# Kernel optimization log

Measured on AMD Instinct MI355X. Metric: run time of the kernel, lower is better.

Reference implementation:

```python
import jax, jax.numpy as jnp
import numpy as np

WIDTH = 64
HEIGHT = 64
FEAT = 128
LAT = 64
NUM_SLOTS = 7


def pixel_coords(img_size):
    g = jnp.linspace(-1.0, 1.0, img_size)
    g1, g2 = jnp.meshgrid(g, g, indexing='ij')  # matches torch.meshgrid default
    return jnp.stack([g1, g2], axis=0)[None]  # (1, 2, S, S)


def clamp_pg(x, lo, hi):
    # clamp that preserves gradients (straight-through)
    return x + jax.lax.stop_gradient(jnp.clip(x, lo, hi) - x)


def setup_inputs() -> dict:
    key = jax.random.key(0)
    k0, k1, k2, k3 = jax.random.split(key, 4)
    bs = 64
    x = jax.random.normal(k0, (bs, FEAT, WIDTH, HEIGHT), jnp.float32)
    rand_pixel = jax.random.uniform(k1, (bs, 1, WIDTH, HEIGHT), jnp.float32)
    conv_w = jax.random.normal(k2, (LAT, FEAT), jnp.float32) / np.sqrt(FEAT)
    conv_b = jax.random.normal(k3, (LAT,), jnp.float32) * 0.01
    gate = jnp.asarray(0.5, jnp.float32)  # ScalarGate parameter (nonzero so c_f is non-degenerate)
    # laplacian kernel: sigma_init = 1 / (sqrt(num_slots) * log 2)
    log_sigma = jnp.asarray(np.log(1.0 / (np.sqrt(NUM_SLOTS) * np.log(2.0))), jnp.float32)
    return {'x': x, 'rand_pixel': rand_pixel, 'conv_w': conv_w, 'conv_b': conv_b,
            'gate': gate, 'log_sigma': log_sigma, 'num_cl_steps': 6}


def _forward(x, rand_pixel, conv_w, conv_b, gate, log_sigma, num_cl_steps):
    bs = x.shape[0]
    # SemiConv: gated 1x1 conv + fixed uv coordinate channels
    out = gate * (jnp.einsum('of,bfhw->bohw', conv_w, x) + conv_b[None, :, None, None])
    uv = jnp.concatenate([jnp.zeros((1, LAT - 2, WIDTH, HEIGHT), out.dtype),
                          pixel_coords(WIDTH).astype(out.dtype)], axis=1)
    c_f = out + uv                      # (bs, LAT, W, H)
    delta = out[:, -2:]                 # (bs, 2, W, H)
    sigma = jnp.exp(log_sigma)
    c_flat = c_f.reshape(bs, LAT, -1)   # (bs, LAT, W*H)
    b_idx = jnp.arange(bs)
    log_s0 = jnp.zeros((bs, 1, WIDTH, HEIGHT), c_f.dtype)

    def step(log_s, _):
        # interpolate-to-same-size is identity -> scope = exp(log_s)
        probs = (rand_pixel * jnp.exp(log_s)).reshape(bs, -1)
        idx = jnp.argmax(probs, axis=1)                 # (bs,)
        seed = c_flat[b_idx, :, idx]                    # (bs, LAT)
        diff = c_f - seed[:, :, None, None]
        dist = jnp.sqrt(clamp_pg((diff ** 2).sum(1), 1e-10, 1e10))  # euclidian (laplacian kernel)
        alpha = jnp.exp(-dist / sigma)[:, None]         # (bs, 1, W, H)
        alpha = clamp_pg(alpha, 0.01, 0.99)
        log_m = log_s + jnp.log(alpha)
        new_log_s = log_s + jnp.log1p(-alpha)
        return new_log_s, (log_m, new_log_s, seed)

    log_s_final, (log_m_steps, log_s_steps, seeds) = jax.lax.scan(
        step, log_s0, None, length=num_cl_steps)
    # log_m_k has num_cl_steps masks plus the final scope appended
    log_m_k = jnp.concatenate([log_m_steps, log_s_final[None]], axis=0)
    log_s_k = jnp.concatenate([log_s0[None], log_s_steps], axis=0)
    return log_m_k, log_s_k, c_f, delta, seeds


def reference(x, rand_pixel, conv_w, conv_b, gate, log_sigma, num_cl_steps):
    return _forward(x, rand_pixel, conv_w, conv_b, gate, log_sigma, num_cl_steps)
```

## Files before the change

kernel.cpp:

```cpp
#include <hip/hip_runtime.h>
#include <hip/hip_bf16.h>

#define NPIX 4096
#define FEAT 128
#define LAT 64
#define BS 64
#define NSTEPS 6

#define OFF_LOGM  0u
#define OFF_LOGS  1835008u
#define OFF_CF    3670016u
#define OFF_DELTA 20447232u
#define OFF_SEEDS 20971520u

typedef float f32x4 __attribute__((ext_vector_type(4)));
typedef short s16x8 __attribute__((ext_vector_type(8)));
typedef short s16x4 __attribute__((ext_vector_type(4)));

__device__ __forceinline__ void amax_comb(float& bv, int& bi, float v, int i) {
    if (v > bv || (v == bv && i < bi)) { bv = v; bi = i; }
}

__device__ __forceinline__ short f2bf_rne(float r) {
    __hip_bfloat16 h = __float2bfloat16(r);
    return __builtin_bit_cast(short, h);
}

__device__ __forceinline__ void split2(float v, short& hi, short& lo) {
    unsigned u = __builtin_bit_cast(unsigned, v);
    hi = (short)(u >> 16);
    float hf = __builtin_bit_cast(float, u & 0xFFFF0000u);
    lo = f2bf_rne(v - hf);
}

__device__ __forceinline__ void transpose4(float4& v, int b) {
    float4 w;
    w.x = __shfl_xor(v.x, 1, 64); w.y = __shfl_xor(v.y, 1, 64);
    w.z = __shfl_xor(v.z, 1, 64); w.w = __shfl_xor(v.w, 1, 64);
    float4 u;
    if ((b & 1) == 0) u = make_float4(v.x, w.x, v.z, w.z);
    else              u = make_float4(w.y, v.y, w.w, v.w);
    float4 w2;
    w2.x = __shfl_xor(u.x, 2, 64); w2.y = __shfl_xor(u.y, 2, 64);
    w2.z = __shfl_xor(u.z, 2, 64); w2.w = __shfl_xor(u.w, 2, 64);
    if ((b & 2) == 0) v = make_float4(u.x, u.y, w2.x, w2.y);
    else              v = make_float4(w2.z, w2.w, u.z, u.w);
}

__global__ void prep_w(const float* __restrict__ w, const float* __restrict__ gate_p,
                       short* __restrict__ gwh, short* __restrict__ gwl)
{
    int i = blockIdx.x * 256 + threadIdx.x;
    float v = gate_p[0] * w[i];
    short h, l; split2(v, h, l);
    gwh[i] = h; gwl[i] = l;
}

template<bool PRE>
__global__ __launch_bounds__(256, PRE ? 4 : 2) void conv_mfma(
    const float* __restrict__ x, const float* __restrict__ rand_pixel,
    const float* __restrict__ w, const float* __restrict__ bias,
    const float* __restrict__ gate_p, float* __restrict__ out,
    float* __restrict__ pval, int* __restrict__ pidx, int* __restrict__ cnt,
    const short* __restrict__ gwh, const short* __restrict__ gwl)
{
    __shared__ __align__(16) short Xhi[256][36];
    __shared__ __align__(16) short Xlo[256][36];
    __shared__ __align__(16) short Whi[PRE ? 1 : 64][PRE ? 1 : 136];
    __shared__ __align__(16) short Wlo[PRE ? 1 : 64][PRE ? 1 : 136];
    __shared__ float sbias[64];

    const int tid  = threadIdx.x;
    const int b    = blockIdx.x >> 4;
    const int tile = blockIdx.x & 15;
    const int p0   = tile * 256;
    const int lane = tid & 63;
    const int wv   = tid >> 6;
    const int l15  = lane & 15;
    const int lg   = lane >> 4;

    if (tile == 0 && wv == 0 && lane < 8) cnt[b * 8 + lane] = 0;

    if constexpr (!PRE) {
        const float gate = gate_p[0];
        #pragma unroll
        for (int i = 0; i < 8; ++i) {
            int q = i * 256 + tid;
            int o = q >> 5;
            int f = (q & 31) * 4;
            float4 wq = *(const float4*)(w + o * 128 + f);
            short h0, l0, h1, l1, h2, l2, h3, l3;
            split2(gate * wq.x, h0, l0);
            split2(gate * wq.y, h1, l1);
            split2(gate * wq.z, h2, l2);
            split2(gate * wq.w, h3, l3);
            *(short4*)&Whi[o][f] = make_short4(h0, h1, h2, h3);
            *(short4*)&Wlo[o][f] = make_short4(l0, l1, l2, l3);
        }
    }
    if (tid < 64) sbias[tid] = gate_p[0] * bias[tid];

    f32x4 acc[4][4];
    #pragma unroll
    for (int og = 0; og < 4; ++og)
        #pragma unroll
        for (int pg = 0; pg < 4; ++pg)
            acc[og][pg] = (f32x4){0.f, 0.f, 0.f, 0.f};

    const float* xb = x + (size_t)b * FEAT * NPIX + p0;

    for (int kc = 0; kc < 4; ++kc) {
        __syncthreads();
        const float* xc = xb + (size_t)(kc * 32) * NPIX + (tid & ~3);
        #pragma unroll
        for (int i = 0; i < 8; ++i) {
            float4 v = *(const float4*)(xc + (size_t)(i * 4 + (tid & 3)) * NPIX);
            transpose4(v, tid & 3);
            short h0, l0, h1, l1, h2, l2, h3, l3;
            split2(v.x, h0, l0);
            split2(v.y, h1, l1);
            split2(v.z, h2, l2);
            split2(v.w, h3, l3);
            *(short4*)&Xhi[tid][i * 4] = make_short4(h0, h1, h2, h3);
            *(short4*)&Xlo[tid][i * 4] = make_short4(l0, l1, l2, l3);
        }
        __syncthreads();

        s16x8 Ah[4], Al[4];
        #pragma unroll
        for (int og = 0; og < 4; ++og) {
            if constexpr (PRE) {
                Ah[og] = *(const s16x8*)&gwh[(og * 16 + l15) * 128 + kc * 32 + lg * 8];
                Al[og] = *(const s16x8*)&gwl[(og * 16 + l15) * 128 + kc * 32 + lg * 8];
            } else {
                Ah[og] = *(const s16x8*)&Whi[og * 16 + l15][kc * 32 + lg * 8];
                Al[og] = *(const s16x8*)&Wlo[og * 16 + l15][kc * 32 + lg * 8];
            }
        }

        #pragma unroll
        for (int pg = 0; pg < 4; ++pg) {
            int pxl = wv * 64 + pg * 16 + l15;
            const short* ph = &Xhi[pxl][lg * 8];
            const short* pl = &Xlo[pxl][lg * 8];
            s16x4 h0 = *(const s16x4*)ph, h1 = *(const s16x4*)(ph + 4);
            s16x4 q0 = *(const s16x4*)pl, q1 = *(const s16x4*)(pl + 4);
            s16x8 Bh = {h0[0], h0[1], h0[2], h0[3], h1[0], h1[1], h1[2], h1[3]};
            s16x8 Bl = {q0[0], q0[1], q0[2], q0[3], q1[0], q1[1], q1[2], q1[3]};
            #pragma unroll
            for (int og = 0; og < 4; ++og) {
                acc[og][pg] = __builtin_amdgcn_mfma_f32_16x16x32_bf16(Ah[og], Bh, acc[og][pg], 0, 0, 0);
                acc[og][pg] = __builtin_amdgcn_mfma_f32_16x16x32_bf16(Ah[og], Bl, acc[og][pg], 0, 0, 0);
                acc[og][pg] = __builtin_amdgcn_mfma_f32_16x16x32_bf16(Al[og], Bh, acc[og][pg], 0, 0, 0);
            }
        }
    }

    float* cf = out + OFF_CF + (size_t)b * LAT * NPIX;
    #pragma unroll
    for (int og = 0; og < 4; ++og) {
        #pragma unroll
        for (int pg = 0; pg < 4; ++pg) {
            #pragma unroll
            for (int r = 0; r < 4; ++r) {
                int o = og * 16 + lg * 4 + r;
                int p = p0 + wv * 64 + pg * 16 + l15;
                float v = acc[og][pg][r] + sbias[o];
                if (o == 62) {
                    out[OFF_DELTA + ((size_t)b * 2 + 0) * NPIX + p] = v;
                    v += (float)(-1.0 + 2.0 * (double)(p >> 6) / 63.0);
                } else if (o == 63) {
                    out[OFF_DELTA + ((size_t)b * 2 + 1) * NPIX + p] = v;
                    v += (float)(-1.0 + 2.0 * (double)(p & 63) / 63.0);
                }
                cf[(size_t)o * NPIX + p] = v;
            }
        }
    }

    if (wv == 0) {
        *(float4*)(out + OFF_LOGS + (size_t)b * NPIX + p0 + lane * 4) =
            make_float4(0.f, 0.f, 0.f, 0.f);
        float4 rv = *(const float4*)(rand_pixel + (size_t)b * NPIX + p0 + lane * 4);
        int pb = p0 + lane * 4;
        float bv = rv.x; int bi = pb;
        if (rv.y > bv) { bv = rv.y; bi = pb + 1; }
        if (rv.z > bv) { bv = rv.z; bi = pb + 2; }
        if (rv.w > bv) { bv = rv.w; bi = pb + 3; }
        #pragma unroll
        for (int off = 32; off > 0; off >>= 1) {
            float ov = __shfl_down(bv, off, 64);
            int   oi = __shfl_down(bi, off, 64);
            amax_comb(bv, bi, ov, oi);
        }
        if (lane == 0) { pval[blockIdx.x] = bv; pidx[blockIdx.x] = bi; }
    }
}

#define REP16(OP) OP(0) OP(1) OP(2) OP(3) OP(4) OP(5) OP(6) OP(7) \
                  OP(8) OP(9) OP(10) OP(11) OP(12) OP(13) OP(14) OP(15)

__global__ __launch_bounds__(1024) void steps_fused(
    const float* __restrict__ rand_pixel, const float* __restrict__ log_sigma_p,
    float* __restrict__ out, float* pv, int* pi, int* cnt)
{
    __shared__ float s_mv[16];
    __shared__ int   s_mi[16];
    __shared__ __align__(16) float s_seed[LAT];
    __shared__ float s_rv[16];
    __shared__ int   s_ri[16];

    const int tid  = threadIdx.x;
    const int b    = blockIdx.x >> 2;
    const int tile = blockIdx.x & 3;
    const int p    = tile * 1024 + tid;

    const float* cfb = out + OFF_CF + (size_t)b * LAT * NPIX;

#define DECLR(i) f32x4 r##i;
    REP16(DECLR)
#define LOADR(i) { \
        float4 v = *(const float4*)(cfb + (size_t)(4*i + (tid & 3)) * NPIX + tile * 1024 + (tid & ~3)); \
        transpose4(v, tid & 3); \
        r##i = (f32x4){v.x, v.y, v.z, v.w}; }
    REP16(LOADR)

    f32x4 aq = r0 * r0;
#define SQR(i) aq += r##i * r##i;
    SQR(1) SQR(2) SQR(3) SQR(4) SQR(5) SQR(6) SQR(7)
    SQR(8) SQR(9) SQR(10) SQR(11) SQR(12) SQR(13) SQR(14) SQR(15)
    const float cr2 = aq[0] + aq[1] + aq[2] + aq[3];

    const float rp    = rand_pixel[(size_t)b * NPIX + p];
    const float sigma = expf(log_sigma_p[0]);
    float ls = 0.f;

    #pragma unroll 1
    for (int s = 0; s < NSTEPS; ++s) {
        if (s > 0) {
            if (tid == 0) {
                while (__hip_atomic_load(&cnt[b * 8 + s], __ATOMIC_ACQUIRE,
                                         __HIP_MEMORY_SCOPE_AGENT) < 4)
                    __builtin_amdgcn_s_sleep(2);
            }
            __syncthreads();
        }
        const int nmerge = (s == 0) ? 16 : 4;
        if (tid < nmerge) {
            s_mv[tid] = __hip_atomic_load(&pv[(s * BS + b) * 16 + tid],
                                          __ATOMIC_RELAXED, __HIP_MEMORY_SCOPE_AGENT);
            s_mi[tid] = __hip_atomic_load(&pi[(s * BS + b) * 16 + tid],
                                          __ATOMIC_RELAXED, __HIP_MEMORY_SCOPE_AGENT);
        }
        __syncthreads();

        float bv = -1.0f; int bi = 0;
        for (int k = 0; k < nmerge; ++k) amax_comb(bv, bi, s_mv[k], s_mi[k]);

        if (tid < LAT) s_seed[tid] = cfb[(size_t)tid * NPIX + bi];
        __syncthreads();
        if (tile == 0 && tid < LAT)
            out[OFF_SEEDS + ((size_t)s * BS + b) * LAT + tid] = s_seed[tid];

        f32x4 dacc = (f32x4){0.f, 0.f, 0.f, 0.f};
        f32x4 sacc = (f32x4){0.f, 0.f, 0.f, 0.f};
#define DOT(i) { f32x4 sv = *(const f32x4*)&s_seed[4*i]; dacc += r##i * sv; sacc += sv * sv; }
        REP16(DOT)
        float dot = dacc[0] + dacc[1] + dacc[2] + dacc[3];
        float s2  = sacc[0] + sacc[1] + sacc[2] + sacc[3];
        float d2  = cr2 + s2 - 2.0f * dot;

        float dist  = sqrtf(fminf(fmaxf(d2, 1e-10f), 1e10f));
        float alpha = expf(-dist / sigma);
        alpha = fminf(fmaxf(alpha, 0.01f), 0.99f);
        float lm  = ls + logf(alpha);
        float lsn = ls + log1pf(-alpha);

        out[OFF_LOGM + ((size_t)s * BS + b) * NPIX + p]       = lm;
        out[OFF_LOGS + ((size_t)(s + 1) * BS + b) * NPIX + p] = lsn;
        ls = lsn;

        if (s == NSTEPS - 1) {
            out[OFF_LOGM + ((size_t)NSTEPS * BS + b) * NPIX + p] = lsn;
        } else {
            float prob = rp * expf(lsn);
            int   idx  = p;
            #pragma unroll
            for (int off = 32; off > 0; off >>= 1) {
                float ov = __shfl_down(prob, off, 64);
                int   oi = __shfl_down(idx, off, 64);
                amax_comb(prob, idx, ov, oi);
            }
            int lane = tid & 63, wid = tid >> 6;
            if (lane == 0) { s_rv[wid] = prob; s_ri[wid] = idx; }
            __syncthreads();
            if (tid == 0) {
                float fb = s_rv[0]; int fi = s_ri[0];
                #pragma unroll
                for (int k = 1; k < 16; ++k) amax_comb(fb, fi, s_rv[k], s_ri[k]);
                __hip_atomic_store(&pv[((s + 1) * BS + b) * 16 + tile], fb,
                                   __ATOMIC_RELAXED, __HIP_MEMORY_SCOPE_AGENT);
                __hip_atomic_store(&pi[((s + 1) * BS + b) * 16 + tile], fi,
                                   __ATOMIC_RELAXED, __HIP_MEMORY_SCOPE_AGENT);
                __hip_atomic_fetch_add(&cnt[b * 8 + s + 1], 1,
                                       __ATOMIC_RELEASE, __HIP_MEMORY_SCOPE_AGENT);
            }
        }
    }
}

__global__ __launch_bounds__(1024) void step_kernel(
    const float* __restrict__ rand_pixel, const float* __restrict__ log_sigma_p,
    float* __restrict__ out, float* pv, int* pi, int step)
{
    __shared__ float s_mv[16];
    __shared__ int   s_mi[16];
    __shared__ __align__(16) float s_seed[LAT];
    __shared__ float s_rv[16];
    __shared__ int   s_ri[16];

    const int tid  = threadIdx.x;
    const int b    = blockIdx.x >> 2;
    const int tile = blockIdx.x & 3;
    const int p    = tile * 1024 + tid;

    const float* cfb = out + OFF_CF + (size_t)b * LAT * NPIX;

    const int nmerge = (step == 0) ? 16 : 4;
    if (tid < nmerge) { s_mv[tid] = pv[(step * BS + b) * 16 + tid];
                        s_mi[tid] = pi[(step * BS + b) * 16 + tid]; }
    __syncthreads();
    float bv = -1.0f; int bi = 0;
    for (int k = 0; k < nmerge; ++k) amax_comb(bv, bi, s_mv[k], s_mi[k]);

    if (tid < LAT) s_seed[tid] = cfb[(size_t)tid * NPIX + bi];
    __syncthreads();
    if (tile == 0 && tid < LAT)
        out[OFF_SEEDS + ((size_t)step * BS + b) * LAT + tid] = s_seed[tid];

    float d2 = 0.f;
    #pragma unroll
    for (int c = 0; c < LAT; ++c) {
        float d = cfb[(size_t)c * NPIX + p] - s_seed[c];
        d2 = fmaf(d, d, d2);
    }
    float dist  = sqrtf(fminf(fmaxf(d2, 1e-10f), 1e10f));
    float sigma = expf(log_sigma_p[0]);
    float alpha = expf(-dist / sigma);
    alpha = fminf(fmaxf(alpha, 0.01f), 0.99f);

    float ls  = out[OFF_LOGS + ((size_t)step * BS + b) * NPIX + p];
    float lm  = ls + logf(alpha);
    float lsn = ls + log1pf(-alpha);

    out[OFF_LOGM + ((size_t)step * BS + b) * NPIX + p]       = lm;
    out[OFF_LOGS + ((size_t)(step + 1) * BS + b) * NPIX + p] = lsn;
    if (step == NSTEPS - 1)
        out[OFF_LOGM + ((size_t)NSTEPS * BS + b) * NPIX + p] = lsn;

    if (step < NSTEPS - 1) {
        float prob = rand_pixel[(size_t)b * NPIX + p] * expf(lsn);
        int   idx  = p;
        #pragma unroll
        for (int off = 32; off > 0; off >>= 1) {
            float ov = __shfl_down(prob, off, 64);
            int   oi = __shfl_down(idx, off, 64);
            amax_comb(prob, idx, ov, oi);
        }
        int lane = tid & 63, wid = tid >> 6;
        if (lane == 0) { s_rv[wid] = prob; s_ri[wid] = idx; }
        __syncthreads();
        if (tid == 0) {
            float fb = s_rv[0]; int fi = s_ri[0];
            #pragma unroll
            for (int k = 1; k < 16; ++k) amax_comb(fb, fi, s_rv[k], s_ri[k]);
            pv[((step + 1) * BS + b) * 16 + tile] = fb;
            pi[((step + 1) * BS + b) * 16 + tile] = fi;
        }
    }
}

extern "C" void kernel_launch(void* const* d_in, const int* in_sizes, int n_in,
                              void* d_out, int out_size, void* d_ws, size_t ws_size,
                              hipStream_t stream) {
    const float* x          = (const float*)d_in[0];
    const float* rand_pixel = (const float*)d_in[1];
    const float* w          = (const float*)d_in[2];
    const float* bias       = (const float*)d_in[3];
    const float* gate       = (const float*)d_in[4];
    const float* log_sigma  = (const float*)d_in[5];

    float* out = (float*)d_out;
    float* pv  = (float*)d_ws;
    int*   pi  = (int*)((char*)d_ws + 24576);
    int*   cnt = (int*)((char*)d_ws + 49152);
    short* gwh = (short*)((char*)d_ws + 51200);
    short* gwl = (short*)((char*)d_ws + 67584);

    const bool pre = (ws_size >= 100 * 1024);

    if (pre) {
        prep_w<<<32, 256, 0, stream>>>(w, gate, gwh, gwl);
        conv_mfma<true><<<1024, 256, 0, stream>>>(x, rand_pixel, w, bias, gate, out,
                                                  pv, pi, cnt, gwh, gwl);
    } else {
        conv_mfma<false><<<1024, 256, 0, stream>>>(x, rand_pixel, w, bias, gate, out,
                                                   pv, pi, cnt, nullptr, nullptr);
    }

    const float* a0 = rand_pixel; const float* a1 = log_sigma; float* a2 = out;
    float* a3 = pv; int* a4 = pi; int* a5 = cnt;
    void* kp[6] = {(void*)&a0, (void*)&a1, (void*)&a2, (void*)&a3, (void*)&a4, (void*)&a5};
    hipError_t e = hipLaunchCooperativeKernel((const void*)steps_fused,
                                              dim3(256), dim3(1024), kp, 0, stream);
    if (e != hipSuccess) {
        for (int s = 0; s < NSTEPS; ++s)
            step_kernel<<<256, 1024, 0, stream>>>(rand_pixel, log_sigma, out, pv, pi, s);
    }
}
```

Before: 145.6 us.

## Load conv inputs directly into registers with double-buffered prefetch, drop LDS staging

The conv kernel no longer stages the transposed, hi/lo-split activations through shared memory. Each lane loads its own float4 fragments straight from global memory into a two-deep register buffer, prefetches the next K chunk while the current one is being computed, and does the transpose and bf16 split in registers right before the MFMAs. This removes the per-chunk LDS writes, reads and barriers, at the cost of more registers and a launch bound dropped to 2 waves per SIMD for the prepacked path. The non-prepacked fallback is removed, so the code now assumes the workspace is large enough. The steps kernel also switches its c_f loads to scalar strided loads instead of float4 loads with a shuffle transpose.

```diff
diff --git a/kernel.cpp b/kernel.cpp
--- a/kernel.cpp
+++ b/kernel.cpp
@@ -15,7 +15,6 @@
 
 typedef float f32x4 __attribute__((ext_vector_type(4)));
 typedef short s16x8 __attribute__((ext_vector_type(8)));
-typedef short s16x4 __attribute__((ext_vector_type(4)));
 
 __device__ __forceinline__ void amax_comb(float& bv, int& bi, float v, int i) {
     if (v > bv || (v == bv && i < bi)) { bv = v; bi = i; }
@@ -56,18 +55,13 @@
     gwh[i] = h; gwl[i] = l;
 }
 
-template<bool PRE>
-__global__ __launch_bounds__(256, PRE ? 4 : 2) void conv_mfma(
+__global__ __launch_bounds__(256, 2) void conv_mfma(
     const float* __restrict__ x, const float* __restrict__ rand_pixel,
-    const float* __restrict__ w, const float* __restrict__ bias,
-    const float* __restrict__ gate_p, float* __restrict__ out,
+    const float* __restrict__ bias, const float* __restrict__ gate_p,
+    float* __restrict__ out,
     float* __restrict__ pval, int* __restrict__ pidx, int* __restrict__ cnt,
     const short* __restrict__ gwh, const short* __restrict__ gwl)
 {
-    __shared__ __align__(16) short Xhi[256][36];
-    __shared__ __align__(16) short Xlo[256][36];
-    __shared__ __align__(16) short Whi[PRE ? 1 : 64][PRE ? 1 : 136];
-    __shared__ __align__(16) short Wlo[PRE ? 1 : 64][PRE ? 1 : 136];
     __shared__ float sbias[64];
 
     const int tid  = threadIdx.x;
@@ -78,26 +72,9 @@
     const int wv   = tid >> 6;
     const int l15  = lane & 15;
     const int lg   = lane >> 4;
+    const int j    = l15 & 3;
 
     if (tile == 0 && wv == 0 && lane < 8) cnt[b * 8 + lane] = 0;
-
-    if constexpr (!PRE) {
-        const float gate = gate_p[0];
-        #pragma unroll
-        for (int i = 0; i < 8; ++i) {
-            int q = i * 256 + tid;
-            int o = q >> 5;
-            int f = (q & 31) * 4;
-            float4 wq = *(const float4*)(w + o * 128 + f);
-            short h0, l0, h1, l1, h2, l2, h3, l3;
-            split2(gate * wq.x, h0, l0);
-            split2(gate * wq.y, h1, l1);
-            split2(gate * wq.z, h2, l2);
-            split2(gate * wq.w, h3, l3);
-            *(short4*)&Whi[o][f] = make_short4(h0, h1, h2, h3);
-            *(short4*)&Wlo[o][f] = make_short4(l0, l1, l2, l3);
-        }
-    }
     if (tid < 64) sbias[tid] = gate_p[0] * bias[tid];
 
     f32x4 acc[4][4];
@@ -107,46 +84,52 @@
         for (int pg = 0; pg < 4; ++pg)
             acc[og][pg] = (f32x4){0.f, 0.f, 0.f, 0.f};
 
-    const float* xb = x + (size_t)b * FEAT * NPIX + p0;
-
+    const float* xq = x + (size_t)b * FEAT * NPIX
+                        + (size_t)(lg * 8 + j) * NPIX
+                        + p0 + wv * 64 + (l15 & ~3);
+
+    float4 buf[2][8];
+
+    #pragma unroll
+    for (int i = 0; i < 8; ++i) {
+        int pg = i >> 1, r = i & 1;
+        buf[0][i] = *(const float4*)(xq + (size_t)(r * 4) * NPIX + pg * 16);
+    }
+
+    #pragma unroll
     for (int kc = 0; kc < 4; ++kc) {
-        __syncthreads();
-        const float* xc = xb + (size_t)(kc * 32) * NPIX + (tid & ~3);
-        #pragma unroll
-        for (int i = 0; i < 8; ++i) {
-            float4 v = *(const float4*)(xc + (size_t)(i * 4 + (tid & 3)) * NPIX);
-            transpose4(v, tid & 3);
-            short h0, l0, h1, l1, h2, l2, h3, l3;
-            split2(v.x, h0, l0);
-            split2(v.y, h1, l1);
-            split2(v.z, h2, l2);
-            split2(v.w, h3, l3);
-            *(short4*)&Xhi[tid][i * 4] = make_short4(h0, h1, h2, h3);
-            *(short4*)&Xlo[tid][i * 4] = make_short4(l0, l1, l2, l3);
-        }
-        __syncthreads();
+        const int cur = kc & 1;
+        if (kc < 3) {
+            #pragma unroll
+            for (int i = 0; i < 8; ++i) {
+                int pg = i >> 1, r = i & 1;
+                buf[cur ^ 1][i] = *(const float4*)(xq + (size_t)((kc + 1) * 32 + r * 4) * NPIX + pg * 16);
+            }
+        }
 
         s16x8 Ah[4], Al[4];
         #pragma unroll
         for (int og = 0; og < 4; ++og) {
-            if constexpr (PRE) {
-                Ah[og] = *(const s16x8*)&gwh[(og * 16 + l15) * 128 + kc * 32 + lg * 8];
-                Al[og] = *(const s16x8*)&gwl[(og * 16 + l15) * 128 + kc * 32 + lg * 8];
-            } else {
-                Ah[og] = *(const s16x8*)&Whi[og * 16 + l15][kc * 32 + lg * 8];
-                Al[og] = *(const s16x8*)&Wlo[og * 16 + l15][kc * 32 + lg * 8];
-            }
+            Ah[og] = *(const s16x8*)&gwh[(og * 16 + l15) * 128 + kc * 32 + lg * 8];
+            Al[og] = *(const s16x8*)&gwl[(og * 16 + l15) * 128 + kc * 32 + lg * 8];
         }
 
         #pragma unroll
         for (int pg = 0; pg < 4; ++pg) {
-            int pxl = wv * 64 + pg * 16 + l15;
-            const short* ph = &Xhi[pxl][lg * 8];
-            const short* pl = &Xlo[pxl][lg * 8];
-            s16x4 h0 = *(const s16x4*)ph, h1 = *(const s16x4*)(ph + 4);
-            s16x4 q0 = *(const s16x4*)pl, q1 = *(const s16x4*)(pl + 4);
-            s16x8 Bh = {h0[0], h0[1], h0[2], h0[3], h1[0], h1[1], h1[2], h1[3]};
-            s16x8 Bl = {q0[0], q0[1], q0[2], q0[3], q1[0], q1[1], q1[2], q1[3]};
+            float4 t0 = buf[cur][pg * 2 + 0];
+            float4 t1 = buf[cur][pg * 2 + 1];
+            transpose4(t0, j);
+            transpose4(t1, j);
+            s16x8 Bh, Bl;
+            short h, l;
+            split2(t0.x, h, l); Bh[0] = h; Bl[0] = l;
+            split2(t0.y, h, l); Bh[1] = h; Bl[1] = l;
+            split2(t0.z, h, l); Bh[2] = h; Bl[2] = l;
+            split2(t0.w, h, l); Bh[3] = h; Bl[3] = l;
+            split2(t1.x, h, l); Bh[4] = h; Bl[4] = l;
+            split2(t1.y, h, l); Bh[5] = h; Bl[5] = l;
+            split2(t1.z, h, l); Bh[6] = h; Bl[6] = l;
+            split2(t1.w, h, l); Bh[7] = h; Bl[7] = l;
             #pragma unroll
             for (int og = 0; og < 4; ++og) {
                 acc[og][pg] = __builtin_amdgcn_mfma_f32_16x16x32_bf16(Ah[og], Bh, acc[og][pg], 0, 0, 0);
@@ -155,6 +138,8 @@
             }
         }
     }
+
+    __syncthreads();
 
     float* cf = out + OFF_CF + (size_t)b * LAT * NPIX;
     #pragma unroll
@@ -219,10 +204,8 @@
 
 #define DECLR(i) f32x4 r##i;
     REP16(DECLR)
-#define LOADR(i) { \
-        float4 v = *(const float4*)(cfb + (size_t)(4*i + (tid & 3)) * NPIX + tile * 1024 + (tid & ~3)); \
-        transpose4(v, tid & 3); \
-        r##i = (f32x4){v.x, v.y, v.z, v.w}; }
+#define LOADR(i) r##i = (f32x4){ cfb[(size_t)(4*i+0)*NPIX + p], cfb[(size_t)(4*i+1)*NPIX + p], \
+                                 cfb[(size_t)(4*i+2)*NPIX + p], cfb[(size_t)(4*i+3)*NPIX + p] };
     REP16(LOADR)
 
     f32x4 aq = r0 * r0;
@@ -397,16 +380,9 @@
     short* gwh = (short*)((char*)d_ws + 51200);
     short* gwl = (short*)((char*)d_ws + 67584);
 
-    const bool pre = (ws_size >= 100 * 1024);
-
-    if (pre) {
-        prep_w<<<32, 256, 0, stream>>>(w, gate, gwh, gwl);
-        conv_mfma<true><<<1024, 256, 0, stream>>>(x, rand_pixel, w, bias, gate, out,
-                                                  pv, pi, cnt, gwh, gwl);
-    } else {
-        conv_mfma<false><<<1024, 256, 0, stream>>>(x, rand_pixel, w, bias, gate, out,
-                                                   pv, pi, cnt, nullptr, nullptr);
-    }
+    prep_w<<<32, 256, 0, stream>>>(w, gate, gwh, gwl);
+    conv_mfma<<<1024, 256, 0, stream>>>(x, rand_pixel, bias, gate, out,
+                                        pv, pi, cnt, gwh, gwl);
 
     const float* a0 = rand_pixel; const float* a1 = log_sigma; float* a2 = out;
     float* a3 = pv; int* a4 = pi; int* a5 = cnt;
```

After: 138.5 us. -4.8%, faster.
